# Performance work log

Measured on AMD Instinct MI355X. Metric: run time of the kernel, lower is better.

Reference implementation:

```python
import jax, jax.numpy as jnp
import numpy as np

B_, K_, C_, HID_, T_, H_, W_ = 4, 4096, 384, 1536, 8, 32, 32
L_ = T_ * H_ * W_


def setup_inputs() -> dict:
    key = jax.random.key(0)
    ks = jax.random.split(key, 8)
    x_sparse = jax.random.normal(ks[0], (B_, K_, C_), dtype=jnp.float32)
    # unique, sorted per-batch active-token indices in [0, L)
    perm_keys = jax.random.split(ks[1], B_)
    indices = jax.vmap(lambda k: jnp.sort(jax.random.permutation(k, L_)[:K_]))(perm_keys).astype(jnp.int32)
    std = 0.02
    w1 = jax.random.normal(ks[2], (HID_, C_), dtype=jnp.float32) * std
    b1 = jnp.zeros((HID_,), dtype=jnp.float32)
    dw_w = jax.random.normal(ks[3], (HID_, 1, 3, 3), dtype=jnp.float32) * std  # depthwise OIHW, I=1
    dw_b = jnp.zeros((HID_,), dtype=jnp.float32)
    w2 = jax.random.normal(ks[4], (C_, HID_), dtype=jnp.float32) * std
    b2 = jnp.zeros((C_,), dtype=jnp.float32)
    return {"x_sparse": x_sparse, "indices": indices, "B": B_, "L": L_, "H": H_, "W": W_,
            "w1": w1, "b1": b1, "dw_w": dw_w, "dw_b": dw_b, "w2": w2, "b2": b2}


def reference(x_sparse, indices, B, L, H, W, w1, b1, dw_w, dw_b, w2, b2):
    K = x_sparse.shape[1]
    HID = w1.shape[0]
    T = L // (H * W)
    # sparse fc1: [B,K,C] @ [C,HID]
    h = jnp.einsum('bkc,hc->bkh', x_sparse, w1) + b1
    # scatter active tokens into zero-initialized dense grid [B,L,HID]
    bidx = jnp.arange(B)[:, None]  # [B,1]
    dense = jnp.zeros((B, L, HID), dtype=h.dtype).at[bidx, indices].set(h)
    # dense depthwise 3x3 conv on [B*T, HID, H, W]
    xs = dense.reshape(B * T, H, W, HID).transpose(0, 3, 1, 2)
    xs = jax.lax.conv_general_dilated(
        xs, dw_w, window_strides=(1, 1), padding='SAME',
        feature_group_count=HID,
        dimension_numbers=('NCHW', 'OIHW', 'NCHW')) + dw_b[None, :, None, None]
    flat = xs.transpose(0, 2, 3, 1).reshape(B, L, HID)
    # gather back the active tokens
    g = flat[bidx, indices]  # [B,K,HID]
    g = jax.nn.gelu(g, approximate=False)  # torch nn.GELU default is exact erf
    # sparse fc2: [B,K,HID] @ [HID,C_out]
    out = jnp.einsum('bkh,ch->bkc', g, w2) + b2
    return out
```

## Files before the change

kernel.cpp:

```cpp
#include <hip/hip_runtime.h>
#include <stdint.h>

using u16 = unsigned short;
using u32 = unsigned int;
using f32x4 = __attribute__((ext_vector_type(4))) float;
using s16x8 = __attribute__((ext_vector_type(8))) short;

#define DEVINL __device__ __forceinline__

constexpr int B_ = 4, K_ = 4096, C_ = 384, HID_ = 1536, H_ = 32, W_ = 32, L_ = 8192;
constexpr int M_ = B_ * K_;

DEVINL u16 f2bf(float f) {
    u32 u = __builtin_bit_cast(u32, f);
    u32 r = (u + 0x7FFFu + ((u >> 16) & 1u)) >> 16;
    return (u16)r;
}
DEVINL float bf2f(u16 h) {
    u32 u = ((u32)h) << 16;
    return __builtin_bit_cast(float, u);
}

__global__ __launch_bounds__(256) void convert_x_kernel(const float* __restrict__ x,
                                                        u16* __restrict__ out) {
    const int i = blockIdx.x * 256 + threadIdx.x;
    const float4* p = (const float4*)(x + (size_t)i * 8);
    float4 a = p[0], b = p[1];
    s16x8 o;
    o[0] = (short)f2bf(a.x); o[1] = (short)f2bf(a.y);
    o[2] = (short)f2bf(a.z); o[3] = (short)f2bf(a.w);
    o[4] = (short)f2bf(b.x); o[5] = (short)f2bf(b.y);
    o[6] = (short)f2bf(b.z); o[7] = (short)f2bf(b.w);
    *(s16x8*)(out + (size_t)i * 8) = o;
}

__global__ __launch_bounds__(256) void prep_small_kernel(
    const float* __restrict__ w1, const float* __restrict__ w2,
    const float* __restrict__ dww, const int* __restrict__ indices,
    u16* __restrict__ w1b, u16* __restrict__ w2b,
    float* __restrict__ dwT, int* __restrict__ pos2k) {
    const int i = blockIdx.x * 256 + threadIdx.x;
    if (i < 147456) {
        const float* src = (i < 73728) ? (w1 + (size_t)i * 8) : (w2 + (size_t)(i - 73728) * 8);
        u16* dst = (i < 73728) ? (w1b + (size_t)i * 8) : (w2b + (size_t)(i - 73728) * 8);
        float4 a = ((const float4*)src)[0];
        float4 b = ((const float4*)src)[1];
        s16x8 o;
        o[0] = (short)f2bf(a.x); o[1] = (short)f2bf(a.y);
        o[2] = (short)f2bf(a.z); o[3] = (short)f2bf(a.w);
        o[4] = (short)f2bf(b.x); o[5] = (short)f2bf(b.y);
        o[6] = (short)f2bf(b.z); o[7] = (short)f2bf(b.w);
        *(s16x8*)dst = o;
    } else if (i < 161280) {
        int t = i - 147456;
        int j = t / 1536;
        int hh = t - j * 1536;
        dwT[j * 1536 + hh] = dww[hh * 9 + j];
    } else {
        int t = i - 161280;
        int b = t >> 12;
        pos2k[(b << 13) + indices[t]] = t & 4095;
    }
}

template <bool OUT_BF16, int CB>
__global__ __launch_bounds__(256) void gemm_bt_kernel(
    const u16* __restrict__ A,
    const u16* __restrict__ Bt,
    const float* __restrict__ bias,
    void* __restrict__ Cv,
    int Mdim, int Ndim, int Kdim) {
    constexpr int BK = 32;
    __shared__ u16 As[128 * BK];
    __shared__ u16 Bs[128 * BK];

    const int flat = blockIdx.x;
    const int per = gridDim.x >> 3;
    const int lid = (flat & 7) * per + (flat >> 3);
    const int rb = lid / CB;
    const int cb = lid - rb * CB;
    const int row0 = rb * 128;
    const int col0 = cb * 128;

    const int tid = threadIdx.x;
    const int wave = tid >> 6;
    const int lane = tid & 63;

    const int sr = lane >> 2;
    const int sc = (lane & 3) * 8;

    const int wr = (wave >> 1) * 64;
    const int wc = (wave & 1) * 64;
    const int fq = lane >> 4;
    const int fr = lane & 15;

    f32x4 acc[4][4];
#pragma unroll
    for (int m = 0; m < 4; ++m)
#pragma unroll
        for (int n = 0; n < 4; ++n) acc[m][n] = f32x4{0.f, 0.f, 0.f, 0.f};

    const int ch0 = wave * 2;
    for (int k0 = 0; k0 < Kdim; k0 += BK) {
        __syncthreads();
#pragma unroll
        for (int cc = 0; cc < 2; ++cc) {
            const int ch = ch0 + cc;
            const int r = ch * 16 + sr;
            const u16* gA = A + (size_t)(row0 + r) * Kdim + k0 + sc;
            __builtin_amdgcn_global_load_lds(
                (const __attribute__((address_space(1))) void*)gA,
                (__attribute__((address_space(3))) void*)(As + ch * 512), 16, 0, 0);
            const u16* gB = Bt + (size_t)(col0 + r) * Kdim + k0 + sc;
            __builtin_amdgcn_global_load_lds(
                (const __attribute__((address_space(1))) void*)gB,
                (__attribute__((address_space(3))) void*)(Bs + ch * 512), 16, 0, 0);
        }
        __syncthreads();

        s16x8 af[4], bf_[4];
#pragma unroll
        for (int m = 0; m < 4; ++m)
            af[m] = *(const s16x8*)(As + (wr + m * 16 + fr) * 32 + fq * 8);
#pragma unroll
        for (int n = 0; n < 4; ++n)
            bf_[n] = *(const s16x8*)(Bs + (wc + n * 16 + fr) * 32 + fq * 8);
#pragma unroll
        for (int m = 0; m < 4; ++m)
#pragma unroll
            for (int n = 0; n < 4; ++n)
                acc[m][n] = __builtin_amdgcn_mfma_f32_16x16x32_bf16(af[m], bf_[n], acc[m][n], 0, 0, 0);
    }

#pragma unroll
    for (int n = 0; n < 4; ++n) {
        const int col = col0 + wc + n * 16 + fr;
        const float bv = bias[col];
#pragma unroll
        for (int m = 0; m < 4; ++m) {
            const int rowb = row0 + wr + m * 16 + fq * 4;
#pragma unroll
            for (int j = 0; j < 4; ++j) {
                float v = acc[m][n][j] + bv;
                if constexpr (OUT_BF16)
                    ((u16*)Cv)[(size_t)(rowb + j) * Ndim + col] = f2bf(v);
                else
                    ((float*)Cv)[(size_t)(rowb + j) * Ndim + col] = v;
            }
        }
    }
}

constexpr int TPB_CONV = 8;
__global__ __launch_bounds__(192, 4) void conv_gelu_kernel(
    const u16* __restrict__ h,
    const int* __restrict__ indices,
    const int* __restrict__ pos2k,
    const float* __restrict__ dwT,
    const float* __restrict__ dwb,
    u16* __restrict__ g)
{
    const int flat = blockIdx.x;
    const int lb = (flat & 7) * ((M_ / TPB_CONV) >> 3) + (flat >> 3);
    const int tok0 = lb * TPB_CONV;
    const int c0 = threadIdx.x * 8;

    float wreg[9][8];
#pragma unroll
    for (int j = 0; j < 9; ++j) {
        const float4 w0 = *(const float4*)(dwT + j * 1536 + c0);
        const float4 w1v = *(const float4*)(dwT + j * 1536 + c0 + 4);
        wreg[j][0] = w0.x; wreg[j][1] = w0.y; wreg[j][2] = w0.z; wreg[j][3] = w0.w;
        wreg[j][4] = w1v.x; wreg[j][5] = w1v.y; wreg[j][6] = w1v.z; wreg[j][7] = w1v.w;
    }
    float bs[8];
    {
        const float4 b0 = *(const float4*)(dwb + c0);
        const float4 b1 = *(const float4*)(dwb + c0 + 4);
        bs[0] = b0.x; bs[1] = b0.y; bs[2] = b0.z; bs[3] = b0.w;
        bs[4] = b1.x; bs[5] = b1.y; bs[6] = b1.z; bs[7] = b1.w;
    }

    for (int ti = 0; ti < TPB_CONV; ++ti) {
        const int token = tok0 + ti;
        const int b = token >> 12;
        const int pos = indices[token];
        const int x = pos & 31;
        const int y = (pos >> 5) & 31;
        const int tb = pos & ~1023;

        float acc[8];
#pragma unroll
        for (int q = 0; q < 8; ++q) acc[q] = bs[q];

#pragma unroll
        for (int dy = -1; dy <= 1; ++dy) {
            const int yy = y + dy;
            if (yy < 0 || yy >= 32) continue;
#pragma unroll
            for (int dx = -1; dx <= 1; ++dx) {
                const int xx = x + dx;
                if (xx < 0 || xx >= 32) continue;
                const int np = tb + (yy << 5) + xx;
                const int kp = pos2k[(b << 13) + np];
                if (kp < 0) continue;
                const int j = (dy + 1) * 3 + (dx + 1);
                const s16x8 hv = *(const s16x8*)(h + ((size_t)(b << 12) + kp) * 1536 + c0);
#pragma unroll
                for (int q = 0; q < 8; ++q)
                    acc[q] += bf2f((u16)hv[q]) * wreg[j][q];
            }
        }

        s16x8 o;
#pragma unroll
        for (int q = 0; q < 8; ++q) {
            const float v = acc[q];
            const float gl = 0.5f * v * (1.0f + erff(v * 0.70710678118654752440f));
            o[q] = (short)f2bf(gl);
        }
        *(s16x8*)(g + (size_t)token * 1536 + c0) = o;
    }
}

extern "C" void kernel_launch(void* const* d_in, const int* in_sizes, int n_in,
                              void* d_out, int out_size, void* d_ws, size_t ws_size,
                              hipStream_t stream) {
    (void)in_sizes; (void)n_in; (void)out_size; (void)ws_size;
    const float* x   = (const float*)d_in[0];
    const int* indices = (const int*)d_in[1];
    const float* w1  = (const float*)d_in[6];
    const float* b1  = (const float*)d_in[7];
    const float* dww = (const float*)d_in[8];
    const float* dwb = (const float*)d_in[9];
    const float* w2  = (const float*)d_in[10];
    const float* b2  = (const float*)d_in[11];

    char* ws = (char*)d_ws;
    size_t off = 0;
    auto alloc = [&](size_t bytes) -> void* {
        void* p = ws + off;
        off += (bytes + 255) & ~(size_t)255;
        return p;
    };
    u16*   Abf   = (u16*)alloc((size_t)M_ * C_ * 2);
    u16*   W1b   = (u16*)alloc((size_t)HID_ * C_ * 2);
    u16*   W2b   = (u16*)alloc((size_t)C_ * HID_ * 2);
    float* dwT   = (float*)alloc((size_t)9 * HID_ * 4);
    int*   pos2k = (int*)alloc((size_t)B_ * L_ * 4);
    u16*   hbuf  = (u16*)alloc((size_t)M_ * HID_ * 2);
    u16*   gbuf  = (u16*)alloc((size_t)M_ * HID_ * 2);

    hipMemsetAsync(pos2k, 0xFF, (size_t)B_ * L_ * 4, stream);
    convert_x_kernel<<<3072, 256, 0, stream>>>(x, Abf);
    prep_small_kernel<<<694, 256, 0, stream>>>(w1, w2, dww, indices, W1b, W2b, dwT, pos2k);

    gemm_bt_kernel<true, HID_ / 128><<<(M_ / 128) * (HID_ / 128), 256, 0, stream>>>(
        Abf, W1b, b1, hbuf, M_, HID_, C_);

    conv_gelu_kernel<<<M_ / TPB_CONV, 192, 0, stream>>>(hbuf, indices, pos2k, dwT, dwb, gbuf);

    gemm_bt_kernel<false, C_ / 128><<<(M_ / 128) * (C_ / 128), 256, 0, stream>>>(
        gbuf, W2b, b2, (float*)d_out, M_, C_, HID_);
}
```

Baseline: 217.7 us.

## Split-K the fc2 GEMM with atomics and branchless neighbor gathers in conv

```diff
diff --git a/kernel.cpp b/kernel.cpp
--- a/kernel.cpp
+++ b/kernel.cpp
@@ -38,7 +38,7 @@
     const float* __restrict__ w1, const float* __restrict__ w2,
     const float* __restrict__ dww, const int* __restrict__ indices,
     u16* __restrict__ w1b, u16* __restrict__ w2b,
-    float* __restrict__ dwT, int* __restrict__ pos2k) {
+    float* __restrict__ dwT, int* __restrict__ pos2k, u16* __restrict__ hzero) {
     const int i = blockIdx.x * 256 + threadIdx.x;
     if (i < 147456) {
         const float* src = (i < 73728) ? (w1 + (size_t)i * 8) : (w2 + (size_t)(i - 73728) * 8);
@@ -56,14 +56,18 @@
         int j = t / 1536;
         int hh = t - j * 1536;
         dwT[j * 1536 + hh] = dww[hh * 9 + j];
-    } else {
+    } else if (i < 177664) {
         int t = i - 161280;
         int b = t >> 12;
         pos2k[(b << 13) + indices[t]] = t & 4095;
-    }
-}
-
-template <bool OUT_BF16, int CB>
+    } else if (i < 177856) {
+        int t = i - 177664;
+        s16x8 z = {0, 0, 0, 0, 0, 0, 0, 0};
+        *(s16x8*)(hzero + t * 8) = z;
+    }
+}
+
+template <bool OUT_BF16, int CB, int SPLITK>
 __global__ __launch_bounds__(256) void gemm_bt_kernel(
     const u16* __restrict__ A,
     const u16* __restrict__ Bt,
@@ -76,7 +80,10 @@
 
     const int flat = blockIdx.x;
     const int per = gridDim.x >> 3;
-    const int lid = (flat & 7) * per + (flat >> 3);
+    const int lidf = (flat & 7) * per + (flat >> 3);
+    const int bps = gridDim.x / SPLITK;
+    const int s = (SPLITK > 1) ? (lidf / bps) : 0;
+    const int lid = lidf - s * bps;
     const int rb = lid / CB;
     const int cb = lid - rb * CB;
     const int row0 = rb * 128;
@@ -100,8 +107,10 @@
 #pragma unroll
         for (int n = 0; n < 4; ++n) acc[m][n] = f32x4{0.f, 0.f, 0.f, 0.f};
 
+    const int ksz = Kdim / SPLITK;
+    const int kbeg = s * ksz;
     const int ch0 = wave * 2;
-    for (int k0 = 0; k0 < Kdim; k0 += BK) {
+    for (int k0 = kbeg; k0 < kbeg + ksz; k0 += BK) {
         __syncthreads();
 #pragma unroll
         for (int cc = 0; cc < 2; ++cc) {
@@ -141,11 +150,16 @@
             const int rowb = row0 + wr + m * 16 + fq * 4;
 #pragma unroll
             for (int j = 0; j < 4; ++j) {
-                float v = acc[m][n][j] + bv;
-                if constexpr (OUT_BF16)
-                    ((u16*)Cv)[(size_t)(rowb + j) * Ndim + col] = f2bf(v);
-                else
-                    ((float*)Cv)[(size_t)(rowb + j) * Ndim + col] = v;
+                if constexpr (SPLITK > 1) {
+                    float v = acc[m][n][j] + ((s == 0) ? bv : 0.0f);
+                    unsafeAtomicAdd(&((float*)Cv)[(size_t)(rowb + j) * Ndim + col], v);
+                } else {
+                    float v = acc[m][n][j] + bv;
+                    if constexpr (OUT_BF16)
+                        ((u16*)Cv)[(size_t)(rowb + j) * Ndim + col] = f2bf(v);
+                    else
+                        ((float*)Cv)[(size_t)(rowb + j) * Ndim + col] = v;
+                }
             }
         }
     }
@@ -160,19 +174,36 @@
     const float* __restrict__ dwb,
     u16* __restrict__ g)
 {
+    __shared__ int nbr[TPB_CONV][9];
+
     const int flat = blockIdx.x;
     const int lb = (flat & 7) * ((M_ / TPB_CONV) >> 3) + (flat >> 3);
     const int tok0 = lb * TPB_CONV;
-    const int c0 = threadIdx.x * 8;
-
-    float wreg[9][8];
-#pragma unroll
-    for (int j = 0; j < 9; ++j) {
-        const float4 w0 = *(const float4*)(dwT + j * 1536 + c0);
-        const float4 w1v = *(const float4*)(dwT + j * 1536 + c0 + 4);
-        wreg[j][0] = w0.x; wreg[j][1] = w0.y; wreg[j][2] = w0.z; wreg[j][3] = w0.w;
-        wreg[j][4] = w1v.x; wreg[j][5] = w1v.y; wreg[j][6] = w1v.z; wreg[j][7] = w1v.w;
-    }
+    const int tid = threadIdx.x;
+    const int c0 = tid * 8;
+
+    if (tid < TPB_CONV * 9) {
+        const int t = tid / 9;
+        const int j = tid - t * 9;
+        const int token = tok0 + t;
+        const int b = token >> 12;
+        const int pos = indices[token];
+        const int x = pos & 31;
+        const int y = (pos >> 5) & 31;
+        const int tb = pos & ~1023;
+        const int dy = j / 3 - 1;
+        const int dx = j - (j / 3) * 3 - 1;
+        const int yy = y + dy;
+        const int xx = x + dx;
+        int row = M_;
+        if (yy >= 0 && yy < 32 && xx >= 0 && xx < 32) {
+            const int kp = pos2k[(b << 13) + tb + (yy << 5) + xx];
+            if (kp >= 0) row = (b << 12) + kp;
+        }
+        nbr[t][j] = row;
+    }
+    __syncthreads();
+
     float bs[8];
     {
         const float4 b0 = *(const float4*)(dwb + c0);
@@ -181,35 +212,31 @@
         bs[4] = b1.x; bs[5] = b1.y; bs[6] = b1.z; bs[7] = b1.w;
     }
 
+#pragma unroll 2
     for (int ti = 0; ti < TPB_CONV; ++ti) {
         const int token = tok0 + ti;
-        const int b = token >> 12;
-        const int pos = indices[token];
-        const int x = pos & 31;
-        const int y = (pos >> 5) & 31;
-        const int tb = pos & ~1023;
+
+        s16x8 hv[9];
+#pragma unroll
+        for (int j = 0; j < 9; ++j)
+            hv[j] = *(const s16x8*)(h + (size_t)nbr[ti][j] * 1536 + c0);
 
         float acc[8];
 #pragma unroll
         for (int q = 0; q < 8; ++q) acc[q] = bs[q];
 
 #pragma unroll
-        for (int dy = -1; dy <= 1; ++dy) {
-            const int yy = y + dy;
-            if (yy < 0 || yy >= 32) continue;
-#pragma unroll
-            for (int dx = -1; dx <= 1; ++dx) {
-                const int xx = x + dx;
-                if (xx < 0 || xx >= 32) continue;
-                const int np = tb + (yy << 5) + xx;
-                const int kp = pos2k[(b << 13) + np];
-                if (kp < 0) continue;
-                const int j = (dy + 1) * 3 + (dx + 1);
-                const s16x8 hv = *(const s16x8*)(h + ((size_t)(b << 12) + kp) * 1536 + c0);
-#pragma unroll
-                for (int q = 0; q < 8; ++q)
-                    acc[q] += bf2f((u16)hv[q]) * wreg[j][q];
-            }
+        for (int j = 0; j < 9; ++j) {
+            const float4 w0 = *(const float4*)(dwT + j * 1536 + c0);
+            const float4 w1v = *(const float4*)(dwT + j * 1536 + c0 + 4);
+            acc[0] += bf2f((u16)hv[j][0]) * w0.x;
+            acc[1] += bf2f((u16)hv[j][1]) * w0.y;
+            acc[2] += bf2f((u16)hv[j][2]) * w0.z;
+            acc[3] += bf2f((u16)hv[j][3]) * w0.w;
+            acc[4] += bf2f((u16)hv[j][4]) * w1v.x;
+            acc[5] += bf2f((u16)hv[j][5]) * w1v.y;
+            acc[6] += bf2f((u16)hv[j][6]) * w1v.z;
+            acc[7] += bf2f((u16)hv[j][7]) * w1v.w;
         }
 
         s16x8 o;
@@ -248,18 +275,20 @@
     u16*   W2b   = (u16*)alloc((size_t)C_ * HID_ * 2);
     float* dwT   = (float*)alloc((size_t)9 * HID_ * 4);
     int*   pos2k = (int*)alloc((size_t)B_ * L_ * 4);
-    u16*   hbuf  = (u16*)alloc((size_t)M_ * HID_ * 2);
+    u16*   hbuf  = (u16*)alloc((size_t)(M_ + 1) * HID_ * 2);
     u16*   gbuf  = (u16*)alloc((size_t)M_ * HID_ * 2);
 
     hipMemsetAsync(pos2k, 0xFF, (size_t)B_ * L_ * 4, stream);
+    hipMemsetAsync(d_out, 0, (size_t)M_ * C_ * 4, stream);
     convert_x_kernel<<<3072, 256, 0, stream>>>(x, Abf);
-    prep_small_kernel<<<694, 256, 0, stream>>>(w1, w2, dww, indices, W1b, W2b, dwT, pos2k);
-
-    gemm_bt_kernel<true, HID_ / 128><<<(M_ / 128) * (HID_ / 128), 256, 0, stream>>>(
+    prep_small_kernel<<<695, 256, 0, stream>>>(w1, w2, dww, indices, W1b, W2b, dwT, pos2k,
+                                               hbuf + (size_t)M_ * HID_);
+
+    gemm_bt_kernel<true, HID_ / 128, 1><<<(M_ / 128) * (HID_ / 128), 256, 0, stream>>>(
         Abf, W1b, b1, hbuf, M_, HID_, C_);
 
     conv_gelu_kernel<<<M_ / TPB_CONV, 192, 0, stream>>>(hbuf, indices, pos2k, dwT, dwb, gbuf);
 
-    gemm_bt_kernel<false, C_ / 128><<<(M_ / 128) * (C_ / 128), 256, 0, stream>>>(
+    gemm_bt_kernel<false, C_ / 128, 2><<<(M_ / 128) * (C_ / 128) * 2, 256, 0, stream>>>(
         gbuf, W2b, b2, (float*)d_out, M_, C_, HID_);
 }
```

Result: slower. 239.4 us (+10.0%).
